# Optimization experiments

Measured on AMD Instinct MI355X. Metric: run time of the kernel, lower is better.

Reference implementation:

```python
import jax, jax.numpy as jnp
import numpy as np

B, S, E = 1, 2048, 4096
H, D = 32, 128  # num_heads, head_dim


def setup_inputs() -> dict:
    key = jax.random.key(0)
    k1, k2, k3 = jax.random.split(key, 3)
    hidden_states = jax.random.normal(k1, (B, S, E), dtype=jnp.float32)
    # real RoPE tables (half-rotation / llama-style), base 10000
    inv_freq = 1.0 / (10000.0 ** (np.arange(0, D, 2, dtype=np.float32) / D))  # [D/2]
    pos = np.arange(S, dtype=np.float32)
    freqs = np.outer(pos, inv_freq)                      # [S, D/2]
    emb = np.concatenate([freqs, freqs], axis=-1)        # [S, D]
    cos = jnp.asarray(np.cos(emb), dtype=jnp.float32)
    sin = jnp.asarray(np.sin(emb), dtype=jnp.float32)
    w_pack = jax.random.normal(k2, (3 * E, E), dtype=jnp.float32) * (E ** -0.5)
    w_o = jax.random.normal(k3, (E, E), dtype=jnp.float32) * (E ** -0.5)
    return {"hidden_states": hidden_states, "cos": cos, "sin": sin,
            "w_pack": w_pack, "w_o": w_o}


def _rotate_half(x):
    x1, x2 = jnp.split(x, 2, axis=-1)
    return jnp.concatenate([-x2, x1], axis=-1)


def reference(hidden_states, cos, sin, w_pack, w_o):
    # fused QKV projection (W_pack, no bias)
    qkv = jnp.einsum('bse,fe->bsf', hidden_states, w_pack)      # [B,S,3E]
    q, k, v = jnp.split(qkv, 3, axis=-1)
    q = q.reshape(B, S, H, D)
    k = k.reshape(B, S, H, D)
    v = v.reshape(B, S, H, D)
    # RoPE (7B path; is_13b=False)
    c = cos[None, :, None, :]
    s = sin[None, :, None, :]
    q = q * c + _rotate_half(q) * s
    k = k * c + _rotate_half(k) * s
    # causal attention (prefill, empty past KV cache)
    scale = 1.0 / jnp.sqrt(jnp.asarray(D, dtype=q.dtype))
    scores = jnp.einsum('bqhd,bkhd->bhqk', q, k) * scale        # [B,H,S,S]
    causal = jnp.tril(jnp.ones((S, S), dtype=bool))
    scores = jnp.where(causal[None, None], scores, jnp.asarray(-1e30, scores.dtype))
    probs = jax.nn.softmax(scores, axis=-1)
    attn = jnp.einsum('bhqk,bkhd->bqhd', probs, v)              # [B,S,H,D]
    attn = attn.reshape(B, S, H * D)
    # output projection
    return jnp.einsum('bsf,ef->bse', attn, w_o)
```

## Files before the change

### kernel.cpp

```cpp
#include <hip/hip_runtime.h>

typedef unsigned short u16;
typedef unsigned int   u32;
typedef __attribute__((ext_vector_type(8))) short short8;
typedef __attribute__((ext_vector_type(4))) float f32x4;

__device__ __forceinline__ float b2f(u16 u) {
  union { float f; u32 i; } v; v.i = ((u32)u) << 16; return v.f;
}
__device__ __forceinline__ u16 f2b(float f) {
  union { float f; u32 i; } v; v.f = f;
  u32 r = v.i + 0x7fffu + ((v.i >> 16) & 1u);
  return (u16)(r >> 16);
}

__device__ __forceinline__ void gload_lds16(const void* g, void* l) {
  __builtin_amdgcn_global_load_lds(
      (const __attribute__((address_space(1))) void*)g,
      (__attribute__((address_space(3))) void*)l, 16, 0, 0);
}

template <int N> __device__ __forceinline__ void wait_vmcnt() {
  if constexpr (N == 0)      asm volatile("s_waitcnt vmcnt(0)" ::: "memory");
  else if constexpr (N == 2) asm volatile("s_waitcnt vmcnt(2)" ::: "memory");
  else if constexpr (N == 3) asm volatile("s_waitcnt vmcnt(3)" ::: "memory");
  else if constexpr (N == 6) asm volatile("s_waitcnt vmcnt(6)" ::: "memory");
  else static_assert(N < 0, "unsupported vmcnt literal");
}

__device__ __forceinline__ ushort4 cvt4(float4 v) {
  ushort4 o;
  o.x = f2b(v.x); o.y = f2b(v.y); o.z = f2b(v.z); o.w = f2b(v.w);
  return o;
}

__global__ __launch_bounds__(256) void cvt_hp(const float* __restrict__ hs,
                                              const float* __restrict__ wp,
                                              u16* __restrict__ h_bf,
                                              u16* __restrict__ wp_bf) {
  const long H4 = 2097152, W4 = 12582912;
  for (long i = (long)blockIdx.x * 256 + threadIdx.x; i < H4 + W4;
       i += (long)gridDim.x * 256) {
    if (i < H4)
      ((ushort4*)h_bf)[i] = cvt4(((const float4*)hs)[i]);
    else
      ((ushort4*)wp_bf)[i - H4] = cvt4(((const float4*)wp)[i - H4]);
  }
}

__global__ __launch_bounds__(256) void cvt_bf16(const float* __restrict__ in,
                                                u16* __restrict__ out, int n4) {
  for (long i = (long)blockIdx.x * 256 + threadIdx.x; i < n4; i += (long)gridDim.x * 256)
    ((ushort4*)out)[i] = cvt4(((const float4*)in)[i]);
}

__device__ __forceinline__ short8 frag_ld64(const u16* base, int rbase, int kk,
                                            int fr, int fq) {
  const int r = rbase + fr;
  return *(const short8*)(base + r * 64 + ((((kk << 2) + fq) ^ (r & 7)) << 3));
}

__global__ __launch_bounds__(512, 2) void gemm8p(const u16* __restrict__ A,
                                                 const u16* __restrict__ B,
                                                 u16* __restrict__ Cq,
                                                 u16* __restrict__ VT,
                                                 int M, int N, int K) {
  constexpr int AE = 16384;
  constexpr int BUFSZ = AE + 12288;
  __shared__ u16 lds[2 * BUFSZ];
  const int tid = threadIdx.x;
  const int wid = tid >> 6, lane = tid & 63;
  const int fr = lane & 15, fq = lane >> 4;
  const int mA = (wid >> 2) * 128;
  const int nB = (wid & 3) * 48;

  const int nty = M >> 8;
  const int qx = gridDim.x >> 3;
  const int wg = (blockIdx.x & 7) * qx + (blockIdx.x >> 3);
  const int by = wg % nty, bx = wg / nty;
  const long row0 = (long)by * 256, col0 = (long)bx * 192;

  const int rr8 = tid >> 3;
  const int jl = (tid & 7) ^ (rr8 & 7);
  const u16* gA = A + (row0 + rr8) * (long)K + jl * 8;
  const u16* gB = B + (col0 + rr8) * (long)K + jl * 8;

  f32x4 acc[8][3];
#pragma unroll
  for (int m = 0; m < 8; ++m)
#pragma unroll
    for (int n = 0; n < 3; ++n) acc[m][n] = f32x4{0.f, 0.f, 0.f, 0.f};

  const int NT = K >> 6;

  auto stageA = [&](int i, int t) {
    gload_lds16(gA + (long)(i * 64) * K + (long)t * 64,
                lds + (t & 1) * BUFSZ + (i * 512 + tid) * 8);
  };
  auto stageB = [&](int i, int t) {
    gload_lds16(gB + (long)(i * 64) * K + (long)t * 64,
                lds + (t & 1) * BUFSZ + AE + (i * 512 + tid) * 8);
  };

#pragma unroll
  for (int i = 0; i < 4; ++i) stageA(i, 0);
#pragma unroll
  for (int i = 0; i < 3; ++i) stageB(i, 0);
#pragma unroll
  for (int i = 0; i < 3; ++i) stageB(i, 1);
  wait_vmcnt<3>();
  __builtin_amdgcn_s_barrier();

  for (int t = 0; t < NT; ++t) {
    const u16* SA = lds + (t & 1) * BUFSZ;
    const u16* SB = SA + AE;
    short8 a0[4], a1[4], b0[3], b1[3];

#pragma unroll
    for (int m = 0; m < 4; ++m) a0[m] = frag_ld64(SA, mA + m * 16, 0, fr, fq);
#pragma unroll
    for (int n = 0; n < 3; ++n) b0[n] = frag_ld64(SB, nB + n * 16, 0, fr, fq);
#pragma unroll
    for (int n = 0; n < 3; ++n) b1[n] = frag_ld64(SB, nB + n * 16, 1, fr, fq);
    if (t + 1 < NT) { stageA(0, t + 1); stageA(1, t + 1); }
    __builtin_amdgcn_s_setprio(1);
#pragma unroll
    for (int m = 0; m < 4; ++m)
#pragma unroll
      for (int n = 0; n < 3; ++n)
        acc[m][n] = __builtin_amdgcn_mfma_f32_16x16x32_bf16(a0[m], b0[n], acc[m][n], 0, 0, 0);
    __builtin_amdgcn_s_setprio(0);
    asm volatile("s_waitcnt lgkmcnt(0)" ::: "memory");
    __builtin_amdgcn_s_barrier();

#pragma unroll
    for (int m = 0; m < 4; ++m) a1[m] = frag_ld64(SA, mA + 64 + m * 16, 0, fr, fq);
    if (t + 1 < NT) { stageA(2, t + 1); stageA(3, t + 1); }
    __builtin_amdgcn_s_setprio(1);
#pragma unroll
    for (int m = 0; m < 4; ++m)
#pragma unroll
      for (int n = 0; n < 3; ++n)
        acc[4 + m][n] = __builtin_amdgcn_mfma_f32_16x16x32_bf16(a1[m], b0[n], acc[4 + m][n], 0, 0, 0);
    __builtin_amdgcn_s_setprio(0);
    __builtin_amdgcn_s_barrier();

#pragma unroll
    for (int m = 0; m < 4; ++m) a0[m] = frag_ld64(SA, mA + m * 16, 1, fr, fq);
    if (t + 2 < NT) { stageB(0, t + 2); stageB(1, t + 2); }
    __builtin_amdgcn_s_setprio(1);
#pragma unroll
    for (int m = 0; m < 4; ++m)
#pragma unroll
      for (int n = 0; n < 3; ++n)
        acc[m][n] = __builtin_amdgcn_mfma_f32_16x16x32_bf16(a0[m], b1[n], acc[m][n], 0, 0, 0);
    __builtin_amdgcn_s_setprio(0);
    __builtin_amdgcn_s_barrier();

#pragma unroll
    for (int m = 0; m < 4; ++m) a1[m] = frag_ld64(SA, mA + 64 + m * 16, 1, fr, fq);
    if (t + 2 < NT) stageB(2, t + 2);
    __builtin_amdgcn_s_setprio(1);
#pragma unroll
    for (int m = 0; m < 4; ++m)
#pragma unroll
      for (int n = 0; n < 3; ++n)
        acc[4 + m][n] = __builtin_amdgcn_mfma_f32_16x16x32_bf16(a1[m], b1[n], acc[4 + m][n], 0, 0, 0);
    __builtin_amdgcn_s_setprio(0);
    if (t + 2 < NT) wait_vmcnt<3>();
    else            wait_vmcnt<0>();
    __builtin_amdgcn_s_barrier();
  }

#pragma unroll
  for (int m = 0; m < 8; ++m)
#pragma unroll
    for (int n = 0; n < 3; ++n) {
      const long c = col0 + nB + n * 16 + fr;
      const long rb = row0 + mA + m * 16 + fq * 4;
      if (c >= 8192) {
        ushort4 o;
        o.x = f2b(acc[m][n][0]); o.y = f2b(acc[m][n][1]);
        o.z = f2b(acc[m][n][2]); o.w = f2b(acc[m][n][3]);
        *(ushort4*)(VT + (c - 8192) * 2048 + rb) = o;
      } else {
#pragma unroll
        for (int j = 0; j < 4; ++j) Cq[(rb + j) * N + c] = f2b(acc[m][n][j]);
      }
    }
}

__global__ __launch_bounds__(512, 2) void gemm2_4p(const u16* __restrict__ A,
                                                   const u16* __restrict__ B,
                                                   float* __restrict__ C,
                                                   int M, int N, int K) {
  constexpr int AE = 16384;
  constexpr int BUFSZ = AE + 8192;
  __shared__ u16 lds[2 * BUFSZ];
  const int tid = threadIdx.x;
  const int wid = tid >> 6, lane = tid & 63;
  const int fr = lane & 15, fq = lane >> 4;
  const int mA = (wid >> 2) * 128;
  const int nB = (wid & 3) * 32;

  const int nty = M >> 8;
  const int qx = gridDim.x >> 3;
  const int wg = (blockIdx.x & 7) * qx + (blockIdx.x >> 3);
  const int by = wg % nty, bx = wg / nty;
  const long row0 = (long)by * 256, col0 = (long)bx * 128;

  const int rr8 = tid >> 3;
  const int jl = (tid & 7) ^ (rr8 & 7);
  const u16* gA = A + (row0 + rr8) * (long)K + jl * 8;
  const u16* gB = B + (col0 + rr8) * (long)K + jl * 8;

  f32x4 acc[8][2];
#pragma unroll
  for (int m = 0; m < 8; ++m)
#pragma unroll
    for (int n = 0; n < 2; ++n) acc[m][n] = f32x4{0.f, 0.f, 0.f, 0.f};

  const int NT = K >> 6;

  auto stageA = [&](int i, int t) {
    gload_lds16(gA + (long)(i * 64) * K + (long)t * 64,
                lds + (t & 1) * BUFSZ + (i * 512 + tid) * 8);
  };
  auto stageB = [&](int i, int t) {
    gload_lds16(gB + (long)(i * 64) * K + (long)t * 64,
                lds + (t & 1) * BUFSZ + AE + (i * 512 + tid) * 8);
  };

#pragma unroll
  for (int i = 0; i < 4; ++i) stageA(i, 0);
#pragma unroll
  for (int i = 0; i < 2; ++i) stageB(i, 0);
#pragma unroll
  for (int i = 0; i < 2; ++i) stageB(i, 1);
  wait_vmcnt<2>();
  __builtin_amdgcn_s_barrier();

  for (int t = 0; t < NT; ++t) {
    const u16* SA = lds + (t & 1) * BUFSZ;
    const u16* SB = SA + AE;
    short8 a0[4], a1[4], b0[2], b1[2];

#pragma unroll
    for (int m = 0; m < 4; ++m) a0[m] = frag_ld64(SA, mA + m * 16, 0, fr, fq);
#pragma unroll
    for (int n = 0; n < 2; ++n) b0[n] = frag_ld64(SB, nB + n * 16, 0, fr, fq);
#pragma unroll
    for (int n = 0; n < 2; ++n) b1[n] = frag_ld64(SB, nB + n * 16, 1, fr, fq);
    if (t + 1 < NT) { stageA(0, t + 1); stageA(1, t + 1); }
    __builtin_amdgcn_s_setprio(1);
#pragma unroll
    for (int m = 0; m < 4; ++m)
#pragma unroll
      for (int n = 0; n < 2; ++n)
        acc[m][n] = __builtin_amdgcn_mfma_f32_16x16x32_bf16(a0[m], b0[n], acc[m][n], 0, 0, 0);
    __builtin_amdgcn_s_setprio(0);
    asm volatile("s_waitcnt lgkmcnt(0)" ::: "memory");
    __builtin_amdgcn_s_barrier();

#pragma unroll
    for (int m = 0; m < 4; ++m) a1[m] = frag_ld64(SA, mA + 64 + m * 16, 0, fr, fq);
    if (t + 1 < NT) { stageA(2, t + 1); stageA(3, t + 1); }
    __builtin_amdgcn_s_setprio(1);
#pragma unroll
    for (int m = 0; m < 4; ++m)
#pragma unroll
      for (int n = 0; n < 2; ++n)
        acc[4 + m][n] = __builtin_amdgcn_mfma_f32_16x16x32_bf16(a1[m], b0[n], acc[4 + m][n], 0, 0, 0);
    __builtin_amdgcn_s_setprio(0);
    __builtin_amdgcn_s_barrier();

#pragma unroll
    for (int m = 0; m < 4; ++m) a0[m] = frag_ld64(SA, mA + m * 16, 1, fr, fq);
    if (t + 2 < NT) stageB(0, t + 2);
    __builtin_amdgcn_s_setprio(1);
#pragma unroll
    for (int m = 0; m < 4; ++m)
#pragma unroll
      for (int n = 0; n < 2; ++n)
        acc[m][n] = __builtin_amdgcn_mfma_f32_16x16x32_bf16(a0[m], b1[n], acc[m][n], 0, 0, 0);
    __builtin_amdgcn_s_setprio(0);
    __builtin_amdgcn_s_barrier();

#pragma unroll
    for (int m = 0; m < 4; ++m) a1[m] = frag_ld64(SA, mA + 64 + m * 16, 1, fr, fq);
    if (t + 2 < NT) stageB(1, t + 2);
    __builtin_amdgcn_s_setprio(1);
#pragma unroll
    for (int m = 0; m < 4; ++m)
#pragma unroll
      for (int n = 0; n < 2; ++n)
        acc[4 + m][n] = __builtin_amdgcn_mfma_f32_16x16x32_bf16(a1[m], b1[n], acc[4 + m][n], 0, 0, 0);
    __builtin_amdgcn_s_setprio(0);
    if (t + 2 < NT) wait_vmcnt<2>();
    else            wait_vmcnt<0>();
    __builtin_amdgcn_s_barrier();
  }

#pragma unroll
  for (int m = 0; m < 8; ++m)
#pragma unroll
    for (int n = 0; n < 2; ++n)
#pragma unroll
      for (int j = 0; j < 4; ++j) {
        const long r = row0 + mA + m * 16 + fq * 4 + j;
        const long c = col0 + nB + n * 16 + fr;
        C[r * N + c] = acc[m][n][j];
      }
}

__global__ __launch_bounds__(256) void rope_qk(u16* __restrict__ qkv,
                                               const float* __restrict__ cosb,
                                               const float* __restrict__ sinb) {
  const int idx = blockIdx.x * 256 + threadIdx.x;
  const int dq  = idx & 15;
  const int h   = (idx >> 4) & 31;
  const int seg = (idx >> 9) & 1;
  const int s   = idx >> 10;
  const int d0  = dq * 4;
  u16* base = qkv + (long)s * 12288 + seg * 4096 + h * 128;
  const ushort4 x1 = *(const ushort4*)(base + d0);
  const ushort4 x2 = *(const ushort4*)(base + d0 + 64);
  const float4 c1 = *(const float4*)(cosb + s * 128 + d0);
  const float4 s1 = *(const float4*)(sinb + s * 128 + d0);
  const float4 c2 = *(const float4*)(cosb + s * 128 + d0 + 64);
  const float4 s2 = *(const float4*)(sinb + s * 128 + d0 + 64);
  const float scale = seg ? 1.0f : 0.08838834764831845f;
  float x1f[4] = {b2f(x1.x), b2f(x1.y), b2f(x1.z), b2f(x1.w)};
  float x2f[4] = {b2f(x2.x), b2f(x2.y), b2f(x2.z), b2f(x2.w)};
  const float c1a[4] = {c1.x, c1.y, c1.z, c1.w}, s1a[4] = {s1.x, s1.y, s1.z, s1.w};
  const float c2a[4] = {c2.x, c2.y, c2.z, c2.w}, s2a[4] = {s2.x, s2.y, s2.z, s2.w};
  ushort4 o1, o2;
  u16* o1p = (u16*)&o1; u16* o2p = (u16*)&o2;
#pragma unroll
  for (int j = 0; j < 4; ++j) {
    o1p[j] = f2b((x1f[j] * c1a[j] - x2f[j] * s1a[j]) * scale);
    o2p[j] = f2b((x2f[j] * c2a[j] + x1f[j] * s2a[j]) * scale);
  }
  *(ushort4*)(base + d0) = o1;
  *(ushort4*)(base + d0 + 64) = o2;
}

__global__ __launch_bounds__(256) void attn_fwd(const u16* __restrict__ Qb,
                                                const u16* __restrict__ Kb,
                                                const u16* __restrict__ Vt,
                                                u16* __restrict__ Ob) {
  const int h  = blockIdx.y;
  const int bxr = gridDim.x - 1 - blockIdx.x;
  const int q0 = bxr * 64;
  const int tid = threadIdx.x;
  const int wid = tid >> 6, lane = tid & 63;
  const int fr = lane & 15, fq = lane >> 4;

  __shared__ u16 Ks[2][64 * 128];
  __shared__ u16 Vts[2][128 * 64];
  __shared__ u16 Ps[4][16 * 72];

  auto stage = [&](int t, int buf) {
    const int kv0 = t * 64;
#pragma unroll
    for (int i = 0; i < 4; ++i) {
      const int c = wid * 4 + i;
      {
        const int r = c * 4 + (lane >> 4);
        const int p = lane & 15;
        const int jsrc = p ^ (r & 7);
        gload_lds16(Kb + (long)(kv0 + r) * 12288 + h * 128 + jsrc * 8,
                    (char*)Ks[buf] + c * 1024);
      }
      {
        const int d = c * 8 + (lane >> 3);
        const int p = lane & 7;
        const int jsrc = p ^ (d & 7);
        gload_lds16(Vt + (long)(h * 128 + d) * 2048 + kv0 + jsrc * 8,
                    (char*)Vts[buf] + c * 1024);
      }
    }
  };

  short8 qf[4];
  {
    const long qrow = q0 + wid * 16 + fr;
#pragma unroll
    for (int kk = 0; kk < 4; ++kk)
      qf[kk] = *(const short8*)(Qb + qrow * 12288 + h * 128 + kk * 32 + fq * 8);
  }

  f32x4 Oacc[8];
#pragma unroll
  for (int f = 0; f < 8; ++f) Oacc[f] = f32x4{0.f, 0.f, 0.f, 0.f};
  float mrun[4], lrun[4];
#pragma unroll
  for (int j = 0; j < 4; ++j) { mrun[j] = -1e30f; lrun[j] = 0.f; }

  const int nt = bxr + 1;
  stage(0, 0);
  asm volatile("s_waitcnt vmcnt(0)" ::: "memory");
  __builtin_amdgcn_s_barrier();

  for (int t = 0; t < nt; ++t) {
    const int cur = t & 1;
    const int kv0 = t * 64;
    if (t + 1 < nt) stage(t + 1, cur ^ 1);

    f32x4 S[4];
#pragma unroll
    for (int n = 0; n < 4; ++n) S[n] = f32x4{0.f, 0.f, 0.f, 0.f};
#pragma unroll
    for (int kk = 0; kk < 4; ++kk) {
#pragma unroll
      for (int n = 0; n < 4; ++n) {
        const int r = n * 16 + fr;
        const int p = (kk * 4 + fq) ^ (r & 7);
        short8 kf = *(const short8*)((const char*)Ks[cur] + r * 256 + p * 16);
        S[n] = __builtin_amdgcn_mfma_f32_16x16x32_bf16(qf[kk], kf, S[n], 0, 0, 0);
      }
    }

    float P[4][4];
    float tm[4] = {-1e30f, -1e30f, -1e30f, -1e30f};
#pragma unroll
    for (int n = 0; n < 4; ++n) {
      const int kv = kv0 + n * 16 + fr;
#pragma unroll
      for (int j = 0; j < 4; ++j) {
        const int qi = q0 + wid * 16 + fq * 4 + j;
        const float s = (kv <= qi) ? S[n][j] : -1e30f;
        P[n][j] = s;
        tm[j] = fmaxf(tm[j], s);
      }
    }
#pragma unroll
    for (int j = 0; j < 4; ++j)
#pragma unroll
      for (int msk = 1; msk < 16; msk <<= 1)
        tm[j] = fmaxf(tm[j], __shfl_xor(tm[j], msk));

    float al[4], rs[4];
#pragma unroll
    for (int j = 0; j < 4; ++j) {
      const float mn = fmaxf(mrun[j], tm[j]);
      al[j] = __expf(mrun[j] - mn);
      mrun[j] = mn;
      rs[j] = 0.f;
    }
#pragma unroll
    for (int n = 0; n < 4; ++n)
#pragma unroll
      for (int j = 0; j < 4; ++j) {
        const float p = __expf(P[n][j] - mrun[j]);
        P[n][j] = p;
        rs[j] += p;
      }
#pragma unroll
    for (int j = 0; j < 4; ++j) {
#pragma unroll
      for (int msk = 1; msk < 16; msk <<= 1) rs[j] += __shfl_xor(rs[j], msk);
      lrun[j] = lrun[j] * al[j] + rs[j];
    }
#pragma unroll
    for (int f = 0; f < 8; ++f) {
      f32x4 o = Oacc[f];
#pragma unroll
      for (int j = 0; j < 4; ++j) o[j] *= al[j];
      Oacc[f] = o;
    }

#pragma unroll
    for (int n = 0; n < 4; ++n)
#pragma unroll
      for (int j = 0; j < 4; ++j)
        Ps[wid][(fq * 4 + j) * 72 + n * 16 + fr] = f2b(P[n][j]);

#pragma unroll
    for (int kb = 0; kb < 2; ++kb) {
      short8 pa = *(const short8*)(Ps[wid] + fr * 72 + kb * 32 + fq * 8);
#pragma unroll
      for (int f = 0; f < 8; ++f) {
        const int d = f * 16 + fr;
        const int p = (kb * 4 + fq) ^ (d & 7);
        short8 vf = *(const short8*)((const char*)Vts[cur] + d * 128 + p * 16);
        Oacc[f] = __builtin_amdgcn_mfma_f32_16x16x32_bf16(pa, vf, Oacc[f], 0, 0, 0);
      }
    }
    asm volatile("s_waitcnt vmcnt(0)" ::: "memory");
    __builtin_amdgcn_s_barrier();
  }

#pragma unroll
  for (int j = 0; j < 4; ++j) {
    const float inv = 1.f / lrun[j];
    const long r = q0 + wid * 16 + fq * 4 + j;
#pragma unroll
    for (int f = 0; f < 8; ++f)
      Ob[r * 4096 + h * 128 + f * 16 + fr] = f2b(Oacc[f][j] * inv);
  }
}

extern "C" void kernel_launch(void* const* d_in, const int* in_sizes, int n_in,
                              void* d_out, int out_size, void* d_ws, size_t ws_size,
                              hipStream_t stream) {
  const float* hs   = (const float*)d_in[0];
  const float* cosb = (const float*)d_in[1];
  const float* sinb = (const float*)d_in[2];
  const float* wp   = (const float*)d_in[3];
  const float* wo   = (const float*)d_in[4];
  float* out = (float*)d_out;
  char* ws = (char*)d_ws;

  u16* h_bf  = (u16*)(ws);
  u16* attn  = (u16*)(ws);
  u16* wp_bf = (u16*)(ws + 16777216);
  u16* wo_bf = (u16*)(ws + 16777216);
  u16* qkv   = (u16*)(ws + 121634816);
  u16* vt    = (u16*)(ws + 171966464);

  cvt_hp<<<4096, 256, 0, stream>>>(hs, wp, h_bf, wp_bf);
  gemm8p<<<512, 512, 0, stream>>>(h_bf, wp_bf, qkv, vt, 2048, 12288, 4096);
  cvt_bf16<<<2048, 256, 0, stream>>>(wo, wo_bf, 4194304);
  rope_qk<<<8192, 256, 0, stream>>>(qkv, cosb, sinb);
  attn_fwd<<<dim3(32, 32), 256, 0, stream>>>(qkv, qkv + 4096, vt, attn);
  gemm2_4p<<<256, 512, 0, stream>>>(attn, wo_bf, out, 2048, 4096, 4096);
}
```

Before: 507.7 us.

## Double query tile per block to 128 rows and drop K/V double buffering

Each attention block now handles 128 query rows: every wave owns 32 rows in two 16-row MFMA sub-tiles, so each K and V fragment read from LDS feeds two MFMAs. The grid halves to 16x32 blocks. The K/V prefetch double buffer is replaced by a single buffer, staged and then synchronised on every tile, and waves whose rows lie fully above the causal diagonal skip compute. This raises K/V reuse and cuts global K/V traffic, but it removes the overlap of loads with compute, lowers block count and occupancy, and adds register pressure.

```diff
diff --git a/kernel.cpp b/kernel.cpp
--- a/kernel.cpp
+++ b/kernel.cpp
@@ -351,16 +351,16 @@
                                                 u16* __restrict__ Ob) {
   const int h  = blockIdx.y;
   const int bxr = gridDim.x - 1 - blockIdx.x;
-  const int q0 = bxr * 64;
+  const int q0 = bxr * 128;
   const int tid = threadIdx.x;
   const int wid = tid >> 6, lane = tid & 63;
   const int fr = lane & 15, fq = lane >> 4;
 
-  __shared__ u16 Ks[2][64 * 128];
-  __shared__ u16 Vts[2][128 * 64];
-  __shared__ u16 Ps[4][16 * 72];
-
-  auto stage = [&](int t, int buf) {
+  __shared__ u16 Ks[64 * 128];
+  __shared__ u16 Vts[128 * 64];
+  __shared__ u16 Ps[4][32 * 72];
+
+  auto stage = [&](int t) {
     const int kv0 = t * 64;
 #pragma unroll
     for (int i = 0; i < 4; ++i) {
@@ -370,135 +370,155 @@
         const int p = lane & 15;
         const int jsrc = p ^ (r & 7);
         gload_lds16(Kb + (long)(kv0 + r) * 12288 + h * 128 + jsrc * 8,
-                    (char*)Ks[buf] + c * 1024);
+                    (char*)Ks + c * 1024);
       }
       {
         const int d = c * 8 + (lane >> 3);
         const int p = lane & 7;
         const int jsrc = p ^ (d & 7);
         gload_lds16(Vt + (long)(h * 128 + d) * 2048 + kv0 + jsrc * 8,
-                    (char*)Vts[buf] + c * 1024);
+                    (char*)Vts + c * 1024);
       }
     }
   };
 
-  short8 qf[4];
-  {
-    const long qrow = q0 + wid * 16 + fr;
+  short8 qf[2][4];
+#pragma unroll
+  for (int m = 0; m < 2; ++m) {
+    const long qrow = q0 + wid * 32 + m * 16 + fr;
 #pragma unroll
     for (int kk = 0; kk < 4; ++kk)
-      qf[kk] = *(const short8*)(Qb + qrow * 12288 + h * 128 + kk * 32 + fq * 8);
+      qf[m][kk] = *(const short8*)(Qb + qrow * 12288 + h * 128 + kk * 32 + fq * 8);
   }
 
-  f32x4 Oacc[8];
-#pragma unroll
-  for (int f = 0; f < 8; ++f) Oacc[f] = f32x4{0.f, 0.f, 0.f, 0.f};
-  float mrun[4], lrun[4];
-#pragma unroll
-  for (int j = 0; j < 4; ++j) { mrun[j] = -1e30f; lrun[j] = 0.f; }
-
-  const int nt = bxr + 1;
-  stage(0, 0);
-  asm volatile("s_waitcnt vmcnt(0)" ::: "memory");
-  __builtin_amdgcn_s_barrier();
+  f32x4 Oacc[2][8];
+#pragma unroll
+  for (int m = 0; m < 2; ++m)
+#pragma unroll
+    for (int f = 0; f < 8; ++f) Oacc[m][f] = f32x4{0.f, 0.f, 0.f, 0.f};
+  float mrun[2][4], lrun[2][4];
+#pragma unroll
+  for (int m = 0; m < 2; ++m)
+#pragma unroll
+    for (int j = 0; j < 4; ++j) { mrun[m][j] = -1e30f; lrun[m][j] = 0.f; }
+
+  const int nt = 2 * bxr + 2;
+  const int wq_hi = q0 + wid * 32 + 31;
 
   for (int t = 0; t < nt; ++t) {
-    const int cur = t & 1;
     const int kv0 = t * 64;
-    if (t + 1 < nt) stage(t + 1, cur ^ 1);
-
-    f32x4 S[4];
-#pragma unroll
-    for (int n = 0; n < 4; ++n) S[n] = f32x4{0.f, 0.f, 0.f, 0.f};
-#pragma unroll
-    for (int kk = 0; kk < 4; ++kk) {
-#pragma unroll
-      for (int n = 0; n < 4; ++n) {
-        const int r = n * 16 + fr;
-        const int p = (kk * 4 + fq) ^ (r & 7);
-        short8 kf = *(const short8*)((const char*)Ks[cur] + r * 256 + p * 16);
-        S[n] = __builtin_amdgcn_mfma_f32_16x16x32_bf16(qf[kk], kf, S[n], 0, 0, 0);
+    stage(t);
+    __syncthreads();
+
+    if (kv0 <= wq_hi) {
+      f32x4 S[2][4];
+#pragma unroll
+      for (int m = 0; m < 2; ++m)
+#pragma unroll
+        for (int n = 0; n < 4; ++n) S[m][n] = f32x4{0.f, 0.f, 0.f, 0.f};
+#pragma unroll
+      for (int kk = 0; kk < 4; ++kk) {
+        short8 kf[4];
+#pragma unroll
+        for (int n = 0; n < 4; ++n) {
+          const int r = n * 16 + fr;
+          const int p = (kk * 4 + fq) ^ (r & 7);
+          kf[n] = *(const short8*)((const char*)Ks + r * 256 + p * 16);
+        }
+#pragma unroll
+        for (int m = 0; m < 2; ++m)
+#pragma unroll
+          for (int n = 0; n < 4; ++n)
+            S[m][n] = __builtin_amdgcn_mfma_f32_16x16x32_bf16(qf[m][kk], kf[n], S[m][n], 0, 0, 0);
+      }
+
+      float P[2][4][4];
+#pragma unroll
+      for (int m = 0; m < 2; ++m) {
+        float tm[4] = {-1e30f, -1e30f, -1e30f, -1e30f};
+#pragma unroll
+        for (int n = 0; n < 4; ++n) {
+          const int kv = kv0 + n * 16 + fr;
+#pragma unroll
+          for (int j = 0; j < 4; ++j) {
+            const int qi = q0 + wid * 32 + m * 16 + fq * 4 + j;
+            const float s = (kv <= qi) ? S[m][n][j] : -1e30f;
+            P[m][n][j] = s;
+            tm[j] = fmaxf(tm[j], s);
+          }
+        }
+#pragma unroll
+        for (int j = 0; j < 4; ++j)
+#pragma unroll
+          for (int msk = 1; msk < 16; msk <<= 1)
+            tm[j] = fmaxf(tm[j], __shfl_xor(tm[j], msk));
+
+        float al[4], rs[4];
+#pragma unroll
+        for (int j = 0; j < 4; ++j) {
+          const float mn = fmaxf(mrun[m][j], tm[j]);
+          al[j] = __expf(mrun[m][j] - mn);
+          mrun[m][j] = mn;
+          rs[j] = 0.f;
+        }
+#pragma unroll
+        for (int n = 0; n < 4; ++n)
+#pragma unroll
+          for (int j = 0; j < 4; ++j) {
+            const float p = __expf(P[m][n][j] - mrun[m][j]);
+            P[m][n][j] = p;
+            rs[j] += p;
+          }
+#pragma unroll
+        for (int j = 0; j < 4; ++j) {
+#pragma unroll
+          for (int msk = 1; msk < 16; msk <<= 1) rs[j] += __shfl_xor(rs[j], msk);
+          lrun[m][j] = lrun[m][j] * al[j] + rs[j];
+        }
+#pragma unroll
+        for (int f = 0; f < 8; ++f) {
+          f32x4 o = Oacc[m][f];
+#pragma unroll
+          for (int j = 0; j < 4; ++j) o[j] *= al[j];
+          Oacc[m][f] = o;
+        }
+      }
+
+#pragma unroll
+      for (int m = 0; m < 2; ++m)
+#pragma unroll
+        for (int n = 0; n < 4; ++n)
+#pragma unroll
+          for (int j = 0; j < 4; ++j)
+            Ps[wid][(m * 16 + fq * 4 + j) * 72 + n * 16 + fr] = f2b(P[m][n][j]);
+
+#pragma unroll
+      for (int kb = 0; kb < 2; ++kb) {
+        short8 pa0 = *(const short8*)(Ps[wid] + (fr) * 72 + kb * 32 + fq * 8);
+        short8 pa1 = *(const short8*)(Ps[wid] + (16 + fr) * 72 + kb * 32 + fq * 8);
+#pragma unroll
+        for (int f = 0; f < 8; ++f) {
+          const int d = f * 16 + fr;
+          const int p = (kb * 4 + fq) ^ (d & 7);
+          short8 vf = *(const short8*)((const char*)Vts + d * 128 + p * 16);
+          Oacc[0][f] = __builtin_amdgcn_mfma_f32_16x16x32_bf16(pa0, vf, Oacc[0][f], 0, 0, 0);
+          Oacc[1][f] = __builtin_amdgcn_mfma_f32_16x16x32_bf16(pa1, vf, Oacc[1][f], 0, 0, 0);
+        }
       }
     }
-
-    float P[4][4];
-    float tm[4] = {-1e30f, -1e30f, -1e30f, -1e30f};
-#pragma unroll
-    for (int n = 0; n < 4; ++n) {
-      const int kv = kv0 + n * 16 + fr;
-#pragma unroll
-      for (int j = 0; j < 4; ++j) {
-        const int qi = q0 + wid * 16 + fq * 4 + j;
-        const float s = (kv <= qi) ? S[n][j] : -1e30f;
-        P[n][j] = s;
-        tm[j] = fmaxf(tm[j], s);
-      }
+    __syncthreads();
+  }
+
+#pragma unroll
+  for (int m = 0; m < 2; ++m)
+#pragma unroll
+    for (int j = 0; j < 4; ++j) {
+      const float inv = 1.f / lrun[m][j];
+      const long r = q0 + wid * 32 + m * 16 + fq * 4 + j;
+#pragma unroll
+      for (int f = 0; f < 8; ++f)
+        Ob[r * 4096 + h * 128 + f * 16 + fr] = f2b(Oacc[m][f][j] * inv);
     }
-#pragma unroll
-    for (int j = 0; j < 4; ++j)
-#pragma unroll
-      for (int msk = 1; msk < 16; msk <<= 1)
-        tm[j] = fmaxf(tm[j], __shfl_xor(tm[j], msk));
-
-    float al[4], rs[4];
-#pragma unroll
-    for (int j = 0; j < 4; ++j) {
-      const float mn = fmaxf(mrun[j], tm[j]);
-      al[j] = __expf(mrun[j] - mn);
-      mrun[j] = mn;
-      rs[j] = 0.f;
-    }
-#pragma unroll
-    for (int n = 0; n < 4; ++n)
-#pragma unroll
-      for (int j = 0; j < 4; ++j) {
-        const float p = __expf(P[n][j] - mrun[j]);
-        P[n][j] = p;
-        rs[j] += p;
-      }
-#pragma unroll
-    for (int j = 0; j < 4; ++j) {
-#pragma unroll
-      for (int msk = 1; msk < 16; msk <<= 1) rs[j] += __shfl_xor(rs[j], msk);
-      lrun[j] = lrun[j] * al[j] + rs[j];
-    }
-#pragma unroll
-    for (int f = 0; f < 8; ++f) {
-      f32x4 o = Oacc[f];
-#pragma unroll
-      for (int j = 0; j < 4; ++j) o[j] *= al[j];
-      Oacc[f] = o;
-    }
-
-#pragma unroll
-    for (int n = 0; n < 4; ++n)
-#pragma unroll
-      for (int j = 0; j < 4; ++j)
-        Ps[wid][(fq * 4 + j) * 72 + n * 16 + fr] = f2b(P[n][j]);
-
-#pragma unroll
-    for (int kb = 0; kb < 2; ++kb) {
-      short8 pa = *(const short8*)(Ps[wid] + fr * 72 + kb * 32 + fq * 8);
-#pragma unroll
-      for (int f = 0; f < 8; ++f) {
-        const int d = f * 16 + fr;
-        const int p = (kb * 4 + fq) ^ (d & 7);
-        short8 vf = *(const short8*)((const char*)Vts[cur] + d * 128 + p * 16);
-        Oacc[f] = __builtin_amdgcn_mfma_f32_16x16x32_bf16(pa, vf, Oacc[f], 0, 0, 0);
-      }
-    }
-    asm volatile("s_waitcnt vmcnt(0)" ::: "memory");
-    __builtin_amdgcn_s_barrier();
-  }
-
-#pragma unroll
-  for (int j = 0; j < 4; ++j) {
-    const float inv = 1.f / lrun[j];
-    const long r = q0 + wid * 16 + fq * 4 + j;
-#pragma unroll
-    for (int f = 0; f < 8; ++f)
-      Ob[r * 4096 + h * 128 + f * 16 + fr] = f2b(Oacc[f][j] * inv);
-  }
 }
 
 extern "C" void kernel_launch(void* const* d_in, const int* in_sizes, int n_in,
@@ -523,6 +543,6 @@
   gemm8p<<<512, 512, 0, stream>>>(h_bf, wp_bf, qkv, vt, 2048, 12288, 4096);
   cvt_bf16<<<2048, 256, 0, stream>>>(wo, wo_bf, 4194304);
   rope_qk<<<8192, 256, 0, stream>>>(qkv, cosb, sinb);
-  attn_fwd<<<dim3(32, 32), 256, 0, stream>>>(qkv, qkv + 4096, vt, attn);
+  attn_fwd<<<dim3(16, 32), 256, 0, stream>>>(qkv, qkv + 4096, vt, attn);
   gemm2_4p<<<256, 512, 0, stream>>>(attn, wo_bf, out, 2048, 4096, 4096);
 }
```

After: 542.3 us. +6.8%, slower.
